# Optimization experiments

Measured on AMD Instinct MI355X. Metric: run time of the kernel, lower is better.

The kernel has to match this reference:

```python
import jax, jax.numpy as jnp
import numpy as np

B, T, D, U = 64, 128, 1024, 1024


def setup_inputs() -> dict:
    key = jax.random.key(0)
    k_x, k_r, k_s, k_wi, k_wh = jax.random.split(key, 5)
    x = jax.random.normal(k_x, (B, T, D), dtype=jnp.float32)
    reset = jax.random.randint(k_r, (B, T), 0, 2, dtype=jnp.int32)
    state = jax.random.normal(k_s, (B, T, U), dtype=jnp.float32)
    # hk.GRU params: w_i (input->3*hidden), w_h (hidden->3*hidden), bias (3*hidden)
    w_i = jax.random.normal(k_wi, (D, 3 * U), dtype=jnp.float32) * (1.0 / np.sqrt(D))
    w_h = jax.random.normal(k_wh, (U, 3 * U), dtype=jnp.float32) * (1.0 / np.sqrt(U))
    b = jnp.zeros((3 * U,), dtype=jnp.float32)
    return {"x": x, "reset": reset, "state": state, "w_i": w_i, "w_h": w_h, "b": b}


def reference(x, reset, state, w_i, w_h, b):
    # _prepare_for_rnn merges (B,T)->rows and adds a length-1 time axis, so
    # hk.dynamic_unroll(ResetCore(GRU)) == one ResetCore(GRU) step over B*T rows.
    Bd, Td, Dd = x.shape
    Ud = w_h.shape[0]
    xf = x.reshape(Bd * Td, Dd)                      # [N, D]
    h = state.reshape(Bd * Td, Ud)                   # [N, U]
    should_reset = reset.reshape(Bd * Td, 1).astype(bool)
    # hk.ResetCore: replace state with initial_state (zeros) where reset is set
    h = jnp.where(should_reset, jnp.zeros_like(h), h)
    # hk.GRU step
    gates_x = xf @ w_i                               # [N, 3U]
    zr_x, a_x = gates_x[:, : 2 * Ud], gates_x[:, 2 * Ud :]
    zr = jax.nn.sigmoid(zr_x + h @ w_h[:, : 2 * Ud] + b[: 2 * Ud])
    z, r = zr[:, :Ud], zr[:, Ud:]
    a = jnp.tanh(a_x + (r * h) @ w_h[:, 2 * Ud :] + b[2 * Ud :])
    h_new = (1.0 - z) * h + z * a                    # [N, U]
    out = h_new.reshape(Bd, Td, Ud)                  # _recover_shape
    new_state = h_new.reshape(Bd, Td, Ud)            # _rnn_reshape back to (B,T,U)
    return out, new_state
```

## Files before the change

### kernel.cpp

```cpp
#include <hip/hip_runtime.h>


typedef __attribute__((ext_vector_type(8))) short short8;
typedef __attribute__((ext_vector_type(4))) short short4v;
typedef __attribute__((ext_vector_type(4))) float floatx4;
typedef __attribute__((ext_vector_type(4))) float f32x4;

#define MROWS 8192
#define KTOT 2048
#define NU 1024
#define NKT 32
#define TBUF 32768
#define TLDS (2 * TBUF)

__device__ __forceinline__ short f2bf(float f) {
  unsigned u = __builtin_bit_cast(unsigned, f);
  u += 0x7fffu + ((u >> 16) & 1u);
  return (short)(u >> 16);
}
__device__ __forceinline__ float bf2f(short s) {
  unsigned u = ((unsigned)(unsigned short)s) << 16;
  return __builtin_bit_cast(float, u);
}
__device__ __forceinline__ float sigmoid_f(float v) { return 1.f / (1.f + __expf(-v)); }
__device__ __forceinline__ float tanh_f(float v) {
  float c = fminf(fmaxf(v, -15.f), 15.f);
  float e = __expf(2.f * c);
  return (e - 1.f) / (e + 1.f);
}

typedef __attribute__((address_space(3))) void* lds_vp;
typedef const __attribute__((address_space(1))) void* gbl_vp;
__device__ __forceinline__ void gload16(const void* g, void* lds) {
  __builtin_amdgcn_global_load_lds((gbl_vp)g, (lds_vp)lds, 16, 0, 0);
}

#define MF(a, b, c) __builtin_amdgcn_mfma_f32_16x16x32_bf16(a, b, c, 0, 0, 0)
#define VMCNT(n) asm volatile("s_waitcnt vmcnt(" #n ")" ::: "memory")
#define LGKM0() asm volatile("s_waitcnt lgkmcnt(0)" ::: "memory")
#define TILE_BAR()                  \
  do {                              \
    __builtin_amdgcn_s_barrier();   \
    asm volatile("" ::: "memory");  \
  } while (0)

__global__ __launch_bounds__(256) void prep_kernel(
    const float* __restrict__ w_i, const float* __restrict__ w_h,
    short* __restrict__ Wc, const float* __restrict__ x,
    const int* __restrict__ reset, const float* __restrict__ state,
    short* __restrict__ xhc) {
  __shared__ float tile[32][33];
  const int b = blockIdx.x;
  if (b < 6144) {
    const int kb = (b & 63) * 32;
    const int nb = (b >> 6) * 32;
    const float* src = (kb < 1024) ? w_i : w_h;
    const int kbl = kb & 1023;
    const int tx = threadIdx.x & 31;
    const int ty = threadIdx.x >> 5;
#pragma unroll
    for (int r = 0; r < 32; r += 8)
      tile[ty + r][tx] = src[(size_t)(kbl + ty + r) * 3072 + nb + tx];
    __syncthreads();
#pragma unroll
    for (int r = 0; r < 32; r += 8)
      Wc[(size_t)(nb + ty + r) * KTOT + kb + tx] = f2bf(tile[tx][ty + r]);
  } else {
    const size_t i4 = (size_t)(b - 6144) * 256 + threadIdx.x;
    const size_t e = i4 * 4;
    const int row = (int)(e >> 10);
    const int d = (int)(e & 1023);
    const float hm = reset[row] ? 0.f : 1.f;
    floatx4 fx = *(const floatx4*)(x + e);
    floatx4 fh = *(const floatx4*)(state + e);
    short4v cx, ch;
#pragma unroll
    for (int k = 0; k < 4; ++k) { cx[k] = f2bf(fx[k]); ch[k] = f2bf(fh[k] * hm); }
    *(short4v*)(xhc + (size_t)row * KTOT + d) = cx;
    *(short4v*)(xhc + (size_t)row * KTOT + 1024 + d) = ch;
  }
}

__global__ __launch_bounds__(256, 2) void zr_kernel(
    const short* __restrict__ xhc, const short* __restrict__ Wc,
    const float* __restrict__ bias, float* __restrict__ zbuf,
    short* __restrict__ rh) {
  extern __shared__ char lds[];
  const int tid = threadIdx.x;
  const int wave = tid >> 6, lane = tid & 63;
  const int wm = wave >> 1, wn = wave & 1;
  const int lrow = lane & 15;
  const int g16 = (lane >> 4) << 4;
  const int swz = (lrow & 7) << 4;
  const int srow = lane >> 3;
  const int scol = ((lane & 7) ^ srow) * 8;

  const int xcd = blockIdx.x & 7, bi = blockIdx.x >> 3;
  const int mtile = xcd * 8 + (bi & 7);
  const int ntile = bi >> 3;
  const int m0 = mtile * 128, n0g = ntile * 128;

  const short* aS = xhc + (size_t)(m0 + wave * 32 + srow) * KTOT + scol;
  const short* bS = Wc + (size_t)(n0g + wave * 32 + srow) * KTOT + scol;
  const int dA = wave * 4096;
  const int dB = 16384 + wave * 4096;

  f32x4 acc[4][4];
#pragma unroll
  for (int i = 0; i < 4; ++i)
#pragma unroll
    for (int j = 0; j < 4; ++j) acc[i][j] = (f32x4){0.f, 0.f, 0.f, 0.f};

#define ZR_STAGE(t, bufp)                                                  \
  _Pragma("unroll") for (int g = 0; g < 4; ++g) {                          \
    gload16(aS + (size_t)g * 8 * KTOT + (t) * 64, (bufp) + dA + g * 1024); \
    gload16(bS + (size_t)g * 8 * KTOT + (t) * 64, (bufp) + dB + g * 1024); \
  }

  ZR_STAGE(0, lds);
  ZR_STAGE(1, lds + TBUF);
  VMCNT(8);
  TILE_BAR();

#pragma unroll 2
  for (int t = 0; t < NKT; ++t) {
    char* buf = lds + (t & 1) * TBUF;
    short8 af[2][4], bq[2][4];
#pragma unroll
    for (int ks = 0; ks < 2; ++ks) {
      const int colb = ((ks * 64 + g16) ^ swz);
      const char* pA = buf + (wm * 64 + lrow) * 128 + colb;
      const char* pB = buf + 16384 + (wn * 64 + lrow) * 128 + colb;
#pragma unroll
      for (int i = 0; i < 4; ++i) af[ks][i] = *(const short8*)(pA + i * 2048);
#pragma unroll
      for (int j = 0; j < 4; ++j) bq[ks][j] = *(const short8*)(pB + j * 2048);
    }
    LGKM0();
    TILE_BAR();
    if (t + 2 < NKT) { ZR_STAGE(t + 2, buf); }
    __builtin_amdgcn_s_setprio(1);
#pragma unroll
    for (int ks = 0; ks < 2; ++ks)
#pragma unroll
      for (int i = 0; i < 4; ++i)
#pragma unroll
        for (int j = 0; j < 4; ++j)
          acc[i][j] = MF(af[ks][i], bq[ks][j], acc[i][j]);
    __builtin_amdgcn_s_setprio(0);
    if (t + 2 < NKT) { VMCNT(8); } else { VMCNT(0); }
    TILE_BAR();
  }
#undef ZR_STAGE

  const bool zh = (n0g < 1024);
#pragma unroll
  for (int j = 0; j < 4; ++j) {
    const int gcn = n0g + wn * 64 + j * 16 + lrow;
    const float bv = bias[gcn];
#pragma unroll
    for (int i = 0; i < 4; ++i) {
#pragma unroll
      for (int rg = 0; rg < 4; ++rg) {
        const int gr = m0 + wm * 64 + i * 16 + (lane >> 4) * 4 + rg;
        const float sv = sigmoid_f(acc[i][j][rg] + bv);
        if (zh) {
          zbuf[(size_t)gr * NU + gcn] = sv;
        } else {
          const int u = gcn - 1024;
          const float hv = bf2f(xhc[(size_t)gr * KTOT + 1024 + u]);
          rh[(size_t)gr * NU + u] = f2bf(sv * hv);
        }
      }
    }
  }
}

__global__ __launch_bounds__(256, 2) void cand_kernel(
    const short* __restrict__ xhc, const short* __restrict__ rh,
    const short* __restrict__ Wc, const float* __restrict__ bias,
    const float* zbuf, float* out) {
  extern __shared__ char lds[];
  const int tid = threadIdx.x;
  const int wave = tid >> 6, lane = tid & 63;
  const int wm = wave >> 1, wn = wave & 1;
  const int lrow = lane & 15;
  const int g16 = (lane >> 4) << 4;
  const int swz = (lrow & 7) << 4;
  const int srow = lane >> 3;
  const int scol = ((lane & 7) ^ srow) * 8;

  const int xcd = blockIdx.x & 7, bi = blockIdx.x >> 3;
  const int mtile = xcd * 8 + (bi & 7);
  const int ntile = bi >> 3;
  const int m0 = mtile * 128, n0g = ntile * 128;

  const short* aX = xhc + (size_t)(m0 + wave * 32 + srow) * KTOT + scol;
  const short* aR = rh + (size_t)(m0 + wave * 32 + srow) * NU + scol;
  const short* bS = Wc + (size_t)(2048 + n0g + wave * 32 + srow) * KTOT + scol;
  const int dA = wave * 4096;
  const int dB = 16384 + wave * 4096;

  f32x4 acc[4][4];
#pragma unroll
  for (int i = 0; i < 4; ++i)
#pragma unroll
    for (int j = 0; j < 4; ++j) acc[i][j] = (f32x4){0.f, 0.f, 0.f, 0.f};

#define CD_STAGE(t, bufp)                                                        \
  _Pragma("unroll") for (int g = 0; g < 4; ++g) {                                \
    if ((t) < 16)                                                                \
      gload16(aX + (size_t)g * 8 * KTOT + (t) * 64, (bufp) + dA + g * 1024);     \
    else                                                                         \
      gload16(aR + (size_t)g * 8 * NU + ((t) - 16) * 64, (bufp) + dA + g * 1024);\
    gload16(bS + (size_t)g * 8 * KTOT + (t) * 64, (bufp) + dB + g * 1024);       \
  }

  CD_STAGE(0, lds);
  CD_STAGE(1, lds + TBUF);
  VMCNT(8);
  TILE_BAR();

#pragma unroll 2
  for (int t = 0; t < NKT; ++t) {
    char* buf = lds + (t & 1) * TBUF;
    short8 af[2][4], bq[2][4];
#pragma unroll
    for (int ks = 0; ks < 2; ++ks) {
      const int colb = ((ks * 64 + g16) ^ swz);
      const char* pA = buf + (wm * 64 + lrow) * 128 + colb;
      const char* pB = buf + 16384 + (wn * 64 + lrow) * 128 + colb;
#pragma unroll
      for (int i = 0; i < 4; ++i) af[ks][i] = *(const short8*)(pA + i * 2048);
#pragma unroll
      for (int j = 0; j < 4; ++j) bq[ks][j] = *(const short8*)(pB + j * 2048);
    }
    LGKM0();
    TILE_BAR();
    if (t + 2 < NKT) { CD_STAGE(t + 2, buf); }
    __builtin_amdgcn_s_setprio(1);
#pragma unroll
    for (int ks = 0; ks < 2; ++ks)
#pragma unroll
      for (int i = 0; i < 4; ++i)
#pragma unroll
        for (int j = 0; j < 4; ++j)
          acc[i][j] = MF(af[ks][i], bq[ks][j], acc[i][j]);
    __builtin_amdgcn_s_setprio(0);
    if (t + 2 < NKT) { VMCNT(8); } else { VMCNT(0); }
    TILE_BAR();
  }
#undef CD_STAGE

#pragma unroll
  for (int j = 0; j < 4; ++j) {
    const int gc = n0g + wn * 64 + j * 16 + lrow;
    const float ba = bias[2048 + gc];
#pragma unroll
    for (int i = 0; i < 4; ++i) {
#pragma unroll
      for (int rg = 0; rg < 4; ++rg) {
        const int gr = m0 + wm * 64 + i * 16 + (lane >> 4) * 4 + rg;
        const float av = tanh_f(acc[i][j][rg] + ba);
        const float zv = zbuf[(size_t)gr * NU + gc];
        const float hv = bf2f(xhc[(size_t)gr * KTOT + 1024 + gc]);
        const float hn = (1.f - zv) * hv + zv * av;
        out[(size_t)gr * NU + gc] = hn;
        out[(size_t)MROWS * NU + (size_t)gr * NU + gc] = hn;
      }
    }
  }
}

extern "C" void kernel_launch(void* const* d_in, const int* in_sizes, int n_in,
                              void* d_out, int out_size, void* d_ws, size_t ws_size,
                              hipStream_t stream) {
  const float* x = (const float*)d_in[0];
  const int* reset = (const int*)d_in[1];
  const float* state = (const float*)d_in[2];
  const float* w_i = (const float*)d_in[3];
  const float* w_h = (const float*)d_in[4];
  const float* bias = (const float*)d_in[5];
  float* out = (float*)d_out;

  short* Wc = (short*)d_ws;
  short* xhc = Wc + (size_t)3072 * KTOT;
  short* rh = xhc + (size_t)MROWS * KTOT;
  float* zbuf = out + (size_t)MROWS * NU;

  hipFuncSetAttribute(reinterpret_cast<const void*>(zr_kernel),
                      hipFuncAttributeMaxDynamicSharedMemorySize, TLDS);
  hipFuncSetAttribute(reinterpret_cast<const void*>(cand_kernel),
                      hipFuncAttributeMaxDynamicSharedMemorySize, TLDS);

  prep_kernel<<<dim3(14336), 256, 0, stream>>>(w_i, w_h, Wc, x, reset, state, xhc);

  zr_kernel<<<dim3(1024), 256, TLDS, stream>>>(xhc, Wc, bias, zbuf, rh);
  cand_kernel<<<dim3(512), 256, TLDS, stream>>>(xhc, rh, Wc, bias, zbuf, out);
}
```

Measured before the change: 160.2 us.

## Load GEMM B operand directly into registers, halving LDS staging

Both GEMM kernels now read the weight (B) tiles from global memory straight into register fragments, double-buffered across k-steps, and stage only the A operand through LDS. The LDS buffer shrinks to half. The MFMA work for each step is split around the barrier so the next A stage and the B register prefetch overlap with compute. This removes LDS write/read traffic for B and lowers LDS footprint, which may allow more occupancy. The cost is more VGPR pressure, uncoalesced-ish per-lane 16-byte global loads duplicated across the two wm waves, and a more delicate vmcnt accounting.

```diff
diff --git a/kernel.cpp b/kernel.cpp
--- a/kernel.cpp
+++ b/kernel.cpp
@@ -10,7 +10,7 @@
 #define KTOT 2048
 #define NU 1024
 #define NKT 32
-#define TBUF 32768
+#define TBUF 16384
 #define TLDS (2 * TBUF)
 
 __device__ __forceinline__ short f2bf(float f) {
@@ -101,9 +101,8 @@
   const int m0 = mtile * 128, n0g = ntile * 128;
 
   const short* aS = xhc + (size_t)(m0 + wave * 32 + srow) * KTOT + scol;
-  const short* bS = Wc + (size_t)(n0g + wave * 32 + srow) * KTOT + scol;
+  const short* bR = Wc + (size_t)(n0g + wn * 64 + lrow) * KTOT + ((lane >> 4) << 3);
   const int dA = wave * 4096;
-  const int dB = 16384 + wave * 4096;
 
   f32x4 acc[4][4];
 #pragma unroll
@@ -111,47 +110,59 @@
 #pragma unroll
     for (int j = 0; j < 4; ++j) acc[i][j] = (f32x4){0.f, 0.f, 0.f, 0.f};
 
+  short8 bq0[2][4], bq1[2][4];
+
 #define ZR_STAGE(t, bufp)                                                  \
-  _Pragma("unroll") for (int g = 0; g < 4; ++g) {                          \
-    gload16(aS + (size_t)g * 8 * KTOT + (t) * 64, (bufp) + dA + g * 1024); \
-    gload16(bS + (size_t)g * 8 * KTOT + (t) * 64, (bufp) + dB + g * 1024); \
+  _Pragma("unroll") for (int g = 0; g < 4; ++g)                            \
+    gload16(aS + (size_t)g * 8 * KTOT + (t) * 64, (bufp) + dA + g * 1024);
+
+#define LOADB(tt, B)                                                       \
+  _Pragma("unroll") for (int j = 0; j < 4; ++j)                            \
+    _Pragma("unroll") for (int ks = 0; ks < 2; ++ks)                       \
+      B[ks][j] = *(const short8*)(bR + (size_t)(j * 16) * KTOT +           \
+                                  (tt) * 64 + ks * 32);
+
+#define ZR_BODY(T, BCUR, BNXT)                                             \
+  {                                                                        \
+    char* buf = lds + ((T) & 1) * TBUF;                                    \
+    short8 af[2][4];                                                       \
+    _Pragma("unroll") for (int ks = 0; ks < 2; ++ks) {                     \
+      const int colb = ((ks * 64 + g16) ^ swz);                            \
+      const char* pA = buf + (wm * 64 + lrow) * 128 + colb;                \
+      _Pragma("unroll") for (int i = 0; i < 4; ++i)                        \
+        af[ks][i] = *(const short8*)(pA + i * 2048);                       \
+    }                                                                      \
+    __builtin_amdgcn_s_setprio(1);                                         \
+    _Pragma("unroll") for (int i = 0; i < 4; ++i)                          \
+      _Pragma("unroll") for (int j = 0; j < 4; ++j)                        \
+        acc[i][j] = MF(af[0][i], BCUR[0][j], acc[i][j]);                   \
+    __builtin_amdgcn_s_setprio(0);                                         \
+    LGKM0();                           \
+    TILE_BAR();                    \
+    if ((T) + 2 < NKT) { ZR_STAGE((T) + 2, buf); }                         \
+    if ((T) + 1 < NKT) { LOADB((T) + 1, BNXT); }                           \
+    __builtin_amdgcn_s_setprio(1);                                         \
+    _Pragma("unroll") for (int i = 0; i < 4; ++i)                          \
+      _Pragma("unroll") for (int j = 0; j < 4; ++j)                        \
+        acc[i][j] = MF(af[1][i], BCUR[1][j], acc[i][j]);                   \
+    __builtin_amdgcn_s_setprio(0);                                         \
+    if ((T) + 1 < NKT) { VMCNT(16); }   \
+    TILE_BAR();                                                            \
   }
 
   ZR_STAGE(0, lds);
   ZR_STAGE(1, lds + TBUF);
-  VMCNT(8);
+  LOADB(0, bq0);
+  VMCNT(12);
   TILE_BAR();
 
-#pragma unroll 2
-  for (int t = 0; t < NKT; ++t) {
-    char* buf = lds + (t & 1) * TBUF;
-    short8 af[2][4], bq[2][4];
-#pragma unroll
-    for (int ks = 0; ks < 2; ++ks) {
-      const int colb = ((ks * 64 + g16) ^ swz);
-      const char* pA = buf + (wm * 64 + lrow) * 128 + colb;
-      const char* pB = buf + 16384 + (wn * 64 + lrow) * 128 + colb;
-#pragma unroll
-      for (int i = 0; i < 4; ++i) af[ks][i] = *(const short8*)(pA + i * 2048);
-#pragma unroll
-      for (int j = 0; j < 4; ++j) bq[ks][j] = *(const short8*)(pB + j * 2048);
-    }
-    LGKM0();
-    TILE_BAR();
-    if (t + 2 < NKT) { ZR_STAGE(t + 2, buf); }
-    __builtin_amdgcn_s_setprio(1);
-#pragma unroll
-    for (int ks = 0; ks < 2; ++ks)
-#pragma unroll
-      for (int i = 0; i < 4; ++i)
-#pragma unroll
-        for (int j = 0; j < 4; ++j)
-          acc[i][j] = MF(af[ks][i], bq[ks][j], acc[i][j]);
-    __builtin_amdgcn_s_setprio(0);
-    if (t + 2 < NKT) { VMCNT(8); } else { VMCNT(0); }
-    TILE_BAR();
-  }
+  for (int t = 0; t < NKT; t += 2) {
+    ZR_BODY(t, bq0, bq1);
+    ZR_BODY(t + 1, bq1, bq0);
+  }
+#undef ZR_BODY
 #undef ZR_STAGE
+#undef LOADB
 
   const bool zh = (n0g < 1024);
 #pragma unroll
@@ -197,9 +208,8 @@
 
   const short* aX = xhc + (size_t)(m0 + wave * 32 + srow) * KTOT + scol;
   const short* aR = rh + (size_t)(m0 + wave * 32 + srow) * NU + scol;
-  const short* bS = Wc + (size_t)(2048 + n0g + wave * 32 + srow) * KTOT + scol;
+  const short* bR = Wc + (size_t)(2048 + n0g + wn * 64 + lrow) * KTOT + ((lane >> 4) << 3);
   const int dA = wave * 4096;
-  const int dB = 16384 + wave * 4096;
 
   f32x4 acc[4][4];
 #pragma unroll
@@ -207,50 +217,64 @@
 #pragma unroll
     for (int j = 0; j < 4; ++j) acc[i][j] = (f32x4){0.f, 0.f, 0.f, 0.f};
 
-#define CD_STAGE(t, bufp)                                                        \
-  _Pragma("unroll") for (int g = 0; g < 4; ++g) {                                \
-    if ((t) < 16)                                                                \
-      gload16(aX + (size_t)g * 8 * KTOT + (t) * 64, (bufp) + dA + g * 1024);     \
-    else                                                                         \
-      gload16(aR + (size_t)g * 8 * NU + ((t) - 16) * 64, (bufp) + dA + g * 1024);\
-    gload16(bS + (size_t)g * 8 * KTOT + (t) * 64, (bufp) + dB + g * 1024);       \
+  short8 bq0[2][4], bq1[2][4];
+
+#define CD_STAGE(t, bufp)                                                      \
+  _Pragma("unroll") for (int g = 0; g < 4; ++g) {                              \
+    if ((t) < 16)                                                              \
+      gload16(aX + (size_t)g * 8 * KTOT + (t) * 64, (bufp) + dA + g * 1024);   \
+    else                                                                       \
+      gload16(aR + (size_t)g * 8 * NU + ((t) - 16) * 64,                       \
+              (bufp) + dA + g * 1024);                                         \
+  }
+
+#define LOADB(tt, B)                                                       \
+  _Pragma("unroll") for (int j = 0; j < 4; ++j)                            \
+    _Pragma("unroll") for (int ks = 0; ks < 2; ++ks)                       \
+      B[ks][j] = *(const short8*)(bR + (size_t)(j * 16) * KTOT +           \
+                                  (tt) * 64 + ks * 32);
+
+#define CD_BODY(T, BCUR, BNXT)                                             \
+  {                                                                        \
+    char* buf = lds + ((T) & 1) * TBUF;                                    \
+    short8 af[2][4];                                                       \
+    _Pragma("unroll") for (int ks = 0; ks < 2; ++ks) {                     \
+      const int colb = ((ks * 64 + g16) ^ swz);                            \
+      const char* pA = buf + (wm * 64 + lrow) * 128 + colb;                \
+      _Pragma("unroll") for (int i = 0; i < 4; ++i)                        \
+        af[ks][i] = *(const short8*)(pA + i * 2048);                       \
+    }                                                                      \
+    __builtin_amdgcn_s_setprio(1);                                         \
+    _Pragma("unroll") for (int i = 0; i < 4; ++i)                          \
+      _Pragma("unroll") for (int j = 0; j < 4; ++j)                        \
+        acc[i][j] = MF(af[0][i], BCUR[0][j], acc[i][j]);                   \
+    __builtin_amdgcn_s_setprio(0);                                         \
+    LGKM0();                                                               \
+    TILE_BAR();                                                            \
+    if ((T) + 2 < NKT) { CD_STAGE((T) + 2, buf); }                         \
+    if ((T) + 1 < NKT) { LOADB((T) + 1, BNXT); }                           \
+    __builtin_amdgcn_s_setprio(1);                                         \
+    _Pragma("unroll") for (int i = 0; i < 4; ++i)                          \
+      _Pragma("unroll") for (int j = 0; j < 4; ++j)                        \
+        acc[i][j] = MF(af[1][i], BCUR[1][j], acc[i][j]);                   \
+    __builtin_amdgcn_s_setprio(0);                                         \
+    if ((T) + 1 < NKT) { VMCNT(16); }                                      \
+    TILE_BAR();                                                            \
   }
 
   CD_STAGE(0, lds);
   CD_STAGE(1, lds + TBUF);
-  VMCNT(8);
+  LOADB(0, bq0);
+  VMCNT(12);
   TILE_BAR();
 
-#pragma unroll 2
-  for (int t = 0; t < NKT; ++t) {
-    char* buf = lds + (t & 1) * TBUF;
-    short8 af[2][4], bq[2][4];
-#pragma unroll
-    for (int ks = 0; ks < 2; ++ks) {
-      const int colb = ((ks * 64 + g16) ^ swz);
-      const char* pA = buf + (wm * 64 + lrow) * 128 + colb;
-      const char* pB = buf + 16384 + (wn * 64 + lrow) * 128 + colb;
-#pragma unroll
-      for (int i = 0; i < 4; ++i) af[ks][i] = *(const short8*)(pA + i * 2048);
-#pragma unroll
-      for (int j = 0; j < 4; ++j) bq[ks][j] = *(const short8*)(pB + j * 2048);
-    }
-    LGKM0();
-    TILE_BAR();
-    if (t + 2 < NKT) { CD_STAGE(t + 2, buf); }
-    __builtin_amdgcn_s_setprio(1);
-#pragma unroll
-    for (int ks = 0; ks < 2; ++ks)
-#pragma unroll
-      for (int i = 0; i < 4; ++i)
-#pragma unroll
-        for (int j = 0; j < 4; ++j)
-          acc[i][j] = MF(af[ks][i], bq[ks][j], acc[i][j]);
-    __builtin_amdgcn_s_setprio(0);
-    if (t + 2 < NKT) { VMCNT(8); } else { VMCNT(0); }
-    TILE_BAR();
-  }
+  for (int t = 0; t < NKT; t += 2) {
+    CD_BODY(t, bq0, bq1);
+    CD_BODY(t + 1, bq1, bq0);
+  }
+#undef CD_BODY
 #undef CD_STAGE
+#undef LOADB
 
 #pragma unroll
   for (int j = 0; j < 4; ++j) {
```

Result: slower. 269.3 us (+68.2%).
